# Kernel optimization log

Hardware: AMD Instinct MI355X
Metric: run time of the kernel (lower is better)

Reference implementation:

```python
import jax, jax.numpy as jnp
import numpy as np
from jax import lax

DN = ('NCHW', 'OIHW', 'NCHW')

def conv(x, w, b):
    y = lax.conv_general_dilated(x, w, (1, 1), 'VALID', dimension_numbers=DN)
    return y + b[None, :, None, None]

def maxpool2(x):
    return lax.reduce_window(x, -jnp.inf, lax.max, (1, 1, 2, 2), (1, 1, 2, 2), 'VALID')

def setup_inputs() -> dict:
    key = jax.random.key(0)
    ks = jax.random.split(key, 16)
    s = 0.05
    return {
        'x': jax.random.normal(ks[0], (8192, 1, 28, 28), jnp.float32),
        'kf_w1': jax.random.normal(ks[1], (8, 1, 7, 7), jnp.float32) * s,
        'kf_b1': jax.random.normal(ks[2], (8,), jnp.float32) * s,
        'kf_w2': jax.random.normal(ks[3], (10, 8, 5, 5), jnp.float32) * s,
        'kf_b2': jax.random.normal(ks[4], (10,), jnp.float32) * s,
        'kf_fc1_w': jax.random.normal(ks[5], (32, 90), jnp.float32) * s,
        'kf_fc1_b': jax.random.normal(ks[6], (32,), jnp.float32) * s,
        'kf_fc2_w': jax.random.normal(ks[7], (40, 32), jnp.float32) * s,
        'kf_fc2_b': jax.random.normal(ks[8], (40,), jnp.float32) * s,
        'conv2_w': jax.random.normal(ks[9], (20, 10, 5, 5), jnp.float32) * s,
        'conv2_b': jax.random.normal(ks[10], (20,), jnp.float32) * s,
        'fc1_w': jax.random.normal(ks[11], (50, 320), jnp.float32) * s,
        'fc1_b': jax.random.normal(ks[12], (50,), jnp.float32) * s,
        'fc2_w': jax.random.normal(ks[13], (10, 50), jnp.float32) * s,
        'fc2_b': jax.random.normal(ks[14], (10,), jnp.float32) * s,
    }

def _forward(x, kf_w1, kf_b1, kf_w2, kf_b2, kf_fc1_w, kf_fc1_b, kf_fc2_w, kf_fc2_b,
             conv2_w, conv2_b, fc1_w, fc1_b, fc2_w, fc2_b):
    n = x.shape[0]
    # KernelFinder: conv7 -> pool -> relu -> conv5 -> pool -> relu
    f = jax.nn.relu(maxpool2(conv(x, kf_w1, kf_b1)))        # [N,8,11,11]
    f = jax.nn.relu(maxpool2(conv(f, kf_w2, kf_b2)))        # [N,10,3,3]
    f = f.reshape(n, 90)
    h = jax.nn.relu(f @ kf_fc1_w.T + kf_fc1_b)
    kernels = (h @ kf_fc2_w.T + kf_fc2_b).reshape(n, 10, 1, 2, 2)
    # per-sample dynamic conv: each image gets its own [10,1,2,2] kernel
    def one(img, k):
        return lax.conv_general_dilated(img[None], k, (1, 1), 'VALID',
                                        dimension_numbers=DN)[0]
    y = jax.vmap(one)(x, kernels)                           # [N,10,27,27]
    y = jax.nn.relu(maxpool2(y))                            # [N,10,13,13]
    # dropout2d is identity in eval mode
    y = jax.nn.relu(maxpool2(conv(y, conv2_w, conv2_b)))    # [N,20,4,4]
    y = y.reshape(n, 320)
    y = jax.nn.relu(y @ fc1_w.T + fc1_b)
    # F.dropout identity in eval
    y = y @ fc2_w.T + fc2_b
    return jax.nn.log_softmax(y, axis=1)

def reference(x, kf_w1, kf_b1, kf_w2, kf_b2, kf_fc1_w, kf_fc1_b, kf_fc2_w, kf_fc2_b,
              conv2_w, conv2_b, fc1_w, fc1_b, fc2_w, fc2_b):
    return _forward(x, kf_w1, kf_b1, kf_w2, kf_b2, kf_fc1_w, kf_fc1_b, kf_fc2_w,
                    kf_fc2_b, conv2_w, conv2_b, fc1_w, fc1_b, fc2_w, fc2_b)
```

## Files before the change

kernel.cpp:

```cpp
#include <hip/hip_runtime.h>
#include <math.h>

#define TPB 192

typedef __attribute__((ext_vector_type(8))) short bf16x8;
typedef __attribute__((ext_vector_type(4))) float f32x4;

#define OX    0
#define OXB   784
#define OC7   2720
#define OC1B  5024
#define OC5   784
#define OY2   784
#define OC2S  2720
#define OF    5552
#define OH    5644
#define OK2   5676
#define OP3   0
#define OPF   320
#define OA1   420
#define OZ    472
#define SM_TOT 5716

#define W3U 0
#define W5U 9600
#define W7U 13184
#define WSU_TOT 14208

__device__ __forceinline__ unsigned short f2bf(float f) {
    unsigned int u = __float_as_uint(f);
    u += 0x7FFF + ((u >> 16) & 1);
    return (unsigned short)(u >> 16);
}

__global__ void repack_w(const float* __restrict__ conv2_w,
                         const float* __restrict__ kf_w2,
                         const float* __restrict__ kf_w1,
                         unsigned short* __restrict__ ws)
{
    int i = blockIdx.x * blockDim.x + threadIdx.x;
    if (i < 9600) {
        int g = i / 640, rem = i % 640;
        int oc = rem >> 5, k = rem & 31;
        int kyp = g % 3, kx = g / 3;
        int kyip = k >> 4, ic = k & 15, ky = 2 * kyp + kyip;
        float v = 0.f;
        if (ic < 10 && ky < 5)
            v = conv2_w[(oc * 10 + ic) * 25 + ky * 5 + kx];
        ws[W3U + i] = f2bf(v);
    } else if (i < 13184) {
        int j = i - 9600;
        int s = j >> 9, rem = j & 511;
        int oc = rem >> 5, k = rem & 31;
        int tap = 4 * s + (k >> 3), ic = k & 7;
        float v = 0.f;
        if (oc < 10 && tap < 25)
            v = kf_w2[(oc * 8 + ic) * 25 + tap];
        ws[W5U + j] = f2bf(v);
    } else if (i < WSU_TOT) {
        int j = i - 13184;
        int s = j >> 9, oc = (j >> 5) & 15, k = j & 31;
        int ky = s * 4 + (k >> 3), kx = k & 7;
        float v = 0.f;
        if (oc < 8 && kx < 7 && ky < 7)
            v = kf_w1[oc * 49 + ky * 7 + kx];
        ws[W7U + j] = f2bf(v);
    }
}

__global__ __launch_bounds__(TPB) void fused_forward(
    const float* __restrict__ x,
    const float* __restrict__ kf_w1, const float* __restrict__ kf_b1,
    const float* __restrict__ kf_w2, const float* __restrict__ kf_b2,
    const float* __restrict__ kf_fc1_w, const float* __restrict__ kf_fc1_b,
    const float* __restrict__ kf_fc2_w, const float* __restrict__ kf_fc2_b,
    const float* __restrict__ conv2_w, const float* __restrict__ conv2_b,
    const float* __restrict__ fc1_w, const float* __restrict__ fc1_b,
    const float* __restrict__ fc2_w, const float* __restrict__ fc2_b,
    const unsigned short* __restrict__ wsu,
    float* __restrict__ out)
{
    __shared__ __align__(16) float sm[SM_TOT];
    const int tid = threadIdx.x;
    const int n = blockIdx.x;

    const float bias1 = kf_b1[tid & 7];
    const int l  = tid & 63, wv = tid >> 6;
    const int lm = l & 15, lk = l >> 4;

    bf16x8 A7_0, A7_1;
    {
        const unsigned short* W7 = wsu + W7U;
        A7_0 = *(const bf16x8*)(W7 + lm * 32 + lk * 8);
        A7_1 = *(const bf16x8*)(W7 + 512 + lm * 32 + lk * 8);
    }

    {
        const float4* xg = (const float4*)(x + (long long)n * 784);
        float4* d = (float4*)&sm[OX];
        for (int i = tid; i < 196; i += TPB) d[i] = xg[i];
    }
    __syncthreads();

    {
        unsigned short* xb = (unsigned short*)&sm[OXB];
        #pragma unroll
        for (int i = 0; i < 20; ++i) {
            int e = i * 192 + tid;
            int s = e / 960, rem = e - s * 960;
            int r = rem >> 5, m = rem & 31;
            int c = m + s;
            float v = (r < 28 && c < 28) ? sm[OX + r * 28 + c] : 0.f;
            xb[s * 968 + rem] = f2bf(v);
        }
    }
    __syncthreads();

    for (int g = 0; g < 3; ++g) {
        {
            const unsigned short* xb = (const unsigned short*)&sm[OXB];
            float* C7 = &sm[OC7];
            #pragma unroll
            for (int j = 0; j < 4; ++j) {
                int nn = (wv * 4 + j) * 16 + lm;
                int lr = nn / 24, c = nn - lr * 24;
                int s = c & 3, q = c - s;
                f32x4 acc = {0.f, 0.f, 0.f, 0.f};
                #pragma unroll
                for (int s4 = 0; s4 < 2; ++s4) {
                    int rb = 8 * g + lr + s4 * 4 + lk;
                    rb = rb > 29 ? 29 : rb;
                    const unsigned short* p = xb + s * 968 + rb * 32 + q;
                    short4 lo = *(const short4*)p;
                    short4 hi = *(const short4*)(p + 4);
                    bf16x8 B;
                    B[0] = lo.x; B[1] = lo.y; B[2] = lo.z; B[3] = lo.w;
                    B[4] = hi.x; B[5] = hi.y; B[6] = hi.z; B[7] = hi.w;
                    acc = __builtin_amdgcn_mfma_f32_16x16x32_bf16(
                        s4 ? A7_1 : A7_0, B, acc, 0, 0, 0);
                }
                if (lk < 2)
                    *(f32x4*)(C7 + nn * 12 + lk * 4) = acc;
            }
        }
        __syncthreads();

        if (tid < 176) {
            int oc = tid & 7, qq = tid >> 3;
            int c = qq % 11, plr2 = qq / 11;
            const float* C7 = &sm[OC7];
            unsigned short* c1b = (unsigned short*)&sm[OC1B];
            #pragma unroll
            for (int hh = 0; hh < 2; ++hh) {
                int plr = plr2 + 2 * hh;
                int p = 4 * g + plr;
                if (p < 11) {
                    int nb = (2 * plr) * 24 + 2 * c;
                    float v00 = C7[nb * 12 + oc];
                    float v01 = C7[(nb + 1) * 12 + oc];
                    float v10 = C7[(nb + 24) * 12 + oc];
                    float v11 = C7[(nb + 25) * 12 + oc];
                    float m = fmaxf(fmaxf(v00, v01), fmaxf(v10, v11)) + bias1;
                    c1b[p * 96 + c * 8 + oc] = f2bf(fmaxf(m, 0.f));
                }
            }
        }
        __syncthreads();
    }

    {
        int nn = wv * 16 + lm;
        int nc = nn > 35 ? 35 : nn;
        const int rr = nc / 6, cc = nc - rr * 6;
        const unsigned short* c1b = (const unsigned short*)&sm[OC1B];
        const char* W5 = (const char*)(wsu + W5U);
        f32x4 acc = {0.f, 0.f, 0.f, 0.f};
        #pragma unroll
        for (int s = 0; s < 7; ++s) {
            int tap = 4 * s + lk;
            int ky = (tap * 13) >> 6;
            int kx = tap - ky * 5;
            bf16x8 A = *(const bf16x8*)(W5 + s * 1024 + lm * 64 + lk * 16);
            bf16x8 B = *(const bf16x8*)(c1b + (rr + ky) * 96 + (cc + kx) * 8);
            acc = __builtin_amdgcn_mfma_f32_16x16x32_bf16(A, B, acc, 0, 0, 0);
        }
        *(f32x4*)(&sm[OC5] + nn * 20 + lk * 4) = acc;
    }
    __syncthreads();

    if (tid < 90) {
        int oc = tid % 10, rr = tid / 10;
        int py = rr / 3, px = rr % 3;
        const float* C5 = &sm[OC5];
        int nb = (2 * py) * 6 + 2 * px;
        float v = fmaxf(fmaxf(C5[nb * 20 + oc], C5[(nb + 1) * 20 + oc]),
                        fmaxf(C5[(nb + 6) * 20 + oc], C5[(nb + 7) * 20 + oc]));
        sm[OF + oc * 9 + rr] = fmaxf(v + kf_b2[oc], 0.f);
    }
    __syncthreads();

    if (tid < 32) {
        float acc = kf_fc1_b[tid];
        const float2* wr = (const float2*)&kf_fc1_w[tid * 90];
        const float2* ff = (const float2*)&sm[OF];
        for (int i = 0; i < 45; ++i) {
            float2 wv2 = wr[i], fv = ff[i];
            acc = fmaf(wv2.x, fv.x, acc);
            acc = fmaf(wv2.y, fv.y, acc);
        }
        sm[OH + tid] = fmaxf(acc, 0.f);
    }
    if (tid < 40) {
        float acc = kf_fc2_b[tid];
        const float4* wr = (const float4*)&kf_fc2_w[tid * 32];
        const float4* hh = (const float4*)&sm[OH];
        #pragma unroll
        for (int i = 0; i < 8; ++i) {
            float4 wv2 = wr[i], hv = hh[i];
            acc = fmaf(wv2.x, hv.x, acc);
            acc = fmaf(wv2.y, hv.y, acc);
            acc = fmaf(wv2.z, hv.z, acc);
            acc = fmaf(wv2.w, hv.w, acc);
        }
        sm[OK2 + tid] = acc;
    }
    if (tid >= 64) {
        float4* z4 = (float4*)&sm[OY2];
        for (int i = tid - 64; i < 468; i += 128) z4[i] = float4{0.f, 0.f, 0.f, 0.f};
    }
    __syncthreads();

    if (tid < 120) {
        int oc = tid % 10, py = tid / 10;
        float4 kv = *(const float4*)&sm[OK2 + oc * 4];
        float k0 = kv.x, k1 = kv.y, k2 = kv.z, k3 = kv.w;
        const float* x0 = &sm[OX + 2 * py * 28];
        const float* x1 = x0 + 28;
        const float* x2 = x0 + 56;
        float2 q0 = *(const float2*)&x0[0];
        float2 q1 = *(const float2*)&x1[0];
        float2 q2 = *(const float2*)&x2[0];
        float A0 = q0.x, B0 = q0.y;
        float A1 = q1.x, B1 = q1.y;
        float A2 = q2.x, B2 = q2.y;
        unsigned short* y2 = (unsigned short*)&sm[OY2];
        #pragma unroll
        for (int j = 0; j < 12; ++j) {
            float2 r0 = *(const float2*)&x0[2 * j + 2];
            float2 r1 = *(const float2*)&x1[2 * j + 2];
            float2 r2v = *(const float2*)&x2[2 * j + 2];
            float C0 = r0.x, C1 = r1.x, C2 = r2v.x;
            float c00 = A0 * k0 + B0 * k1 + A1 * k2 + B1 * k3;
            float c01 = B0 * k0 + C0 * k1 + B1 * k2 + C1 * k3;
            float c10 = A1 * k0 + B1 * k1 + A2 * k2 + B2 * k3;
            float c11 = B1 * k0 + C1 * k1 + B2 * k2 + C2 * k3;
            float m = fmaxf(fmaxf(c00, c01), fmaxf(c10, c11));
            y2[py * 288 + j * 24 + oc] = f2bf(fmaxf(m, 0.f));
            A0 = C0; A1 = C1; A2 = C2;
            B0 = r0.y; B1 = r1.y; B2 = r2v.y;
        }
    }
    __syncthreads();

    if (wv < 2) {
        f32x4 a00 = {0.f, 0.f, 0.f, 0.f};
        f32x4 a01 = a00, a10 = a00, a11 = a00;
        const char* W3 = (const char*)(wsu + W3U);
        const int aoff0 = lm * 64 + lk * 16;
        const int oc1 = 16 + (lm < 4 ? lm : 3);
        const int aoff1 = oc1 * 64 + lk * 16;
        const int n0 = wv * 32 + lm;
        const int n1 = n0 + 16;
        const int kyip = l >> 5, icb = (lk & 1) * 8;
        const unsigned short* Y2 = (const unsigned short*)&sm[OY2];
        const int b0 = ((n0 >> 3) + kyip) * 288 + (n0 & 7) * 24 + icb;
        const int b1 = ((n1 >> 3) + kyip) * 288 + (n1 & 7) * 24 + icb;
        #pragma unroll
        for (int p = 0; p < 3; ++p) {
            #pragma unroll
            for (int kx = 0; kx < 5; ++kx) {
                const char* wa = W3 + (kx * 3 + p) * 1280;
                bf16x8 A0 = *(const bf16x8*)(wa + aoff0);
                bf16x8 A1 = *(const bf16x8*)(wa + aoff1);
                const int bo = p * 576 + kx * 24;
                bf16x8 B0 = *(const bf16x8*)(Y2 + b0 + bo);
                bf16x8 B1 = *(const bf16x8*)(Y2 + b1 + bo);
                a00 = __builtin_amdgcn_mfma_f32_16x16x32_bf16(A0, B0, a00, 0, 0, 0);
                a01 = __builtin_amdgcn_mfma_f32_16x16x32_bf16(A0, B1, a01, 0, 0, 0);
                a10 = __builtin_amdgcn_mfma_f32_16x16x32_bf16(A1, B0, a10, 0, 0, 0);
                a11 = __builtin_amdgcn_mfma_f32_16x16x32_bf16(A1, B1, a11, 0, 0, 0);
            }
        }
        float* C = &sm[OC2S];
        *(f32x4*)(C + n0 * 36 + lk * 4)      = a00;
        *(f32x4*)(C + n1 * 36 + lk * 4)      = a01;
        *(f32x4*)(C + n0 * 36 + 16 + lk * 4) = a10;
        *(f32x4*)(C + n1 * 36 + 16 + lk * 4) = a11;
    }
    __syncthreads();

    if (tid < 80) {
        int oc = tid % 20, py = tid / 20;
        float b = conv2_b[oc];
        const float* C = &sm[OC2S];
        #pragma unroll
        for (int px = 0; px < 4; ++px) {
            int n00 = (2 * py) * 8 + 2 * px;
            float c00 = C[n00 * 36 + oc];
            float c01 = C[(n00 + 1) * 36 + oc];
            float c10 = C[(n00 + 8) * 36 + oc];
            float c11 = C[(n00 + 9) * 36 + oc];
            float m = fmaxf(fmaxf(c00, c01), fmaxf(c10, c11)) + b;
            sm[OP3 + oc * 16 + py * 4 + px] = fmaxf(m, 0.f);
        }
    }
    __syncthreads();

    if (tid < 100) {
        int g = tid / 50, o = tid % 50;
        const float4* wr4 = (const float4*)&fc1_w[o * 320 + g * 160];
        const float4* pp4 = (const float4*)&sm[OP3 + g * 160];
        float acc = 0.f;
        for (int i = 0; i < 40; ++i) {
            float4 wv2 = wr4[i], pv = pp4[i];
            acc = fmaf(wv2.x, pv.x, acc);
            acc = fmaf(wv2.y, pv.y, acc);
            acc = fmaf(wv2.z, pv.z, acc);
            acc = fmaf(wv2.w, pv.w, acc);
        }
        sm[OPF + tid] = acc;
    }
    __syncthreads();

    if (tid < 50) {
        float acc = fc1_b[tid] + sm[OPF + tid] + sm[OPF + 50 + tid];
        sm[OA1 + tid] = fmaxf(acc, 0.f);
    }
    if (tid < 10) {
        float acc = fc2_b[tid];
        const float2* wr = (const float2*)&fc2_w[tid * 50];
        #pragma unroll
        for (int i = 0; i < 25; ++i) {
            float2 wv2 = wr[i];
            acc = fmaf(wv2.x, sm[OA1 + 2 * i], acc);
            acc = fmaf(wv2.y, sm[OA1 + 2 * i + 1], acc);
        }
        sm[OZ + tid] = acc;
    }
    if (tid < 10) {
        float m = sm[OZ + 0];
        #pragma unroll
        for (int i = 1; i < 10; ++i) m = fmaxf(m, sm[OZ + i]);
        float s = 0.f;
        #pragma unroll
        for (int i = 0; i < 10; ++i) s += expf(sm[OZ + i] - m);
        out[n * 10 + tid] = sm[OZ + tid] - m - logf(s);
    }
}

extern "C" void kernel_launch(void* const* d_in, const int* in_sizes, int n_in,
                              void* d_out, int out_size, void* d_ws, size_t ws_size,
                              hipStream_t stream) {
    const float* x        = (const float*)d_in[0];
    const float* kf_w1    = (const float*)d_in[1];
    const float* kf_b1    = (const float*)d_in[2];
    const float* kf_w2    = (const float*)d_in[3];
    const float* kf_b2    = (const float*)d_in[4];
    const float* kf_fc1_w = (const float*)d_in[5];
    const float* kf_fc1_b = (const float*)d_in[6];
    const float* kf_fc2_w = (const float*)d_in[7];
    const float* kf_fc2_b = (const float*)d_in[8];
    const float* conv2_w  = (const float*)d_in[9];
    const float* conv2_b  = (const float*)d_in[10];
    const float* fc1_w    = (const float*)d_in[11];
    const float* fc1_b    = (const float*)d_in[12];
    const float* fc2_w    = (const float*)d_in[13];
    const float* fc2_b    = (const float*)d_in[14];

    const int N = in_sizes[0] / 784;

    unsigned short* wsu = (unsigned short*)d_ws;
    repack_w<<<(WSU_TOT + 255) / 256, 256, 0, stream>>>(conv2_w, kf_w2, kf_w1, wsu);

    fused_forward<<<N, TPB, 0, stream>>>(
        x, kf_w1, kf_b1, kf_w2, kf_b2, kf_fc1_w, kf_fc1_b, kf_fc2_w, kf_fc2_b,
        conv2_w, conv2_b, fc1_w, fc1_b, fc2_w, fc2_b, wsu, (float*)d_out);
}
```

Baseline: 217.7 us.

## Fuse maxpool into MFMA epilogues via DPP lane shuffles, drop conv staging buffers

The MFMA column mapping for conv7 and conv5 is reordered so that the four outputs of each 2x2 pool window land in neighbouring lanes (lane xor 1 and xor 8). Pooling then uses DPP max shuffles in registers, with bias, ReLU and bf16 packing applied before results are written straight to shared memory. This removes the C7/C5 staging buffers, the separate pooling passes and several __syncthreads per group, and it shrinks shared memory use, which may raise occupancy. The risk is in the more intricate lane-to-output mapping and in guard conditions that leave some lanes idle.

New measurement: 221.4 us. About the same (+1.7%).

```diff
diff --git a/kernel.cpp b/kernel.cpp
--- a/kernel.cpp
+++ b/kernel.cpp
@@ -8,19 +8,17 @@
 
 #define OX    0
 #define OXB   784
-#define OC7   2720
-#define OC1B  5024
-#define OC5   784
+#define OC1B  2720
 #define OY2   784
+#define OF    3248
+#define OH    3340
+#define OK2   3372
 #define OC2S  2720
-#define OF    5552
-#define OH    5644
-#define OK2   5676
 #define OP3   0
 #define OPF   320
 #define OA1   420
 #define OZ    472
-#define SM_TOT 5716
+#define SM_TOT 5024
 
 #define W3U 0
 #define W5U 9600
@@ -31,6 +29,17 @@
     unsigned int u = __float_as_uint(f);
     u += 0x7FFF + ((u >> 16) & 1);
     return (unsigned short)(u >> 16);
+}
+
+__device__ __forceinline__ float dppmax1(float v) {
+    float o = __int_as_float(__builtin_amdgcn_mov_dpp(
+        __float_as_int(v), 0xB1, 0xF, 0xF, true));
+    return fmaxf(v, o);
+}
+__device__ __forceinline__ float dppmax8(float v) {
+    float o = __int_as_float(__builtin_amdgcn_mov_dpp(
+        __float_as_int(v), 0x128, 0xF, 0xF, true));
+    return fmaxf(v, o);
 }
 
 __global__ void repack_w(const float* __restrict__ conv2_w,
@@ -84,7 +93,6 @@
     const int tid = threadIdx.x;
     const int n = blockIdx.x;
 
-    const float bias1 = kf_b1[tid & 7];
     const int l  = tid & 63, wv = tid >> 6;
     const int lm = l & 15, lk = l >> 4;
 
@@ -94,6 +102,7 @@
         A7_0 = *(const bf16x8*)(W7 + lm * 32 + lk * 8);
         A7_1 = *(const bf16x8*)(W7 + 512 + lm * 32 + lk * 8);
     }
+    float4 b1v = *(const float4*)(kf_b1 + (lk < 2 ? lk : 0) * 4);
 
     {
         const float4* xg = (const float4*)(x + (long long)n * 784);
@@ -116,15 +125,16 @@
     }
     __syncthreads();
 
-    for (int g = 0; g < 3; ++g) {
-        {
-            const unsigned short* xb = (const unsigned short*)&sm[OXB];
-            float* C7 = &sm[OC7];
+    {
+        const unsigned short* xb = (const unsigned short*)&sm[OXB];
+        unsigned short* c1b = (unsigned short*)&sm[OC1B];
+        for (int g = 0; g < 3; ++g) {
             #pragma unroll
             for (int j = 0; j < 4; ++j) {
-                int nn = (wv * 4 + j) * 16 + lm;
-                int lr = nn / 24, c = nn - lr * 24;
-                int s = c & 3, q = c - s;
+                int t = wv * 4 + j;
+                int C = 2 * t + (lm >> 3);
+                int lr = lm & 7;
+                int s = C & 3, q = C - s;
                 f32x4 acc = {0.f, 0.f, 0.f, 0.f};
                 #pragma unroll
                 for (int s4 = 0; s4 < 2; ++s4) {
@@ -139,39 +149,28 @@
                     acc = __builtin_amdgcn_mfma_f32_16x16x32_bf16(
                         s4 ? A7_1 : A7_0, B, acc, 0, 0, 0);
                 }
-                if (lk < 2)
-                    *(f32x4*)(C7 + nn * 12 + lk * 4) = acc;
-            }
-        }
-        __syncthreads();
-
-        if (tid < 176) {
-            int oc = tid & 7, qq = tid >> 3;
-            int c = qq % 11, plr2 = qq / 11;
-            const float* C7 = &sm[OC7];
-            unsigned short* c1b = (unsigned short*)&sm[OC1B];
-            #pragma unroll
-            for (int hh = 0; hh < 2; ++hh) {
-                int plr = plr2 + 2 * hh;
-                int p = 4 * g + plr;
-                if (p < 11) {
-                    int nb = (2 * plr) * 24 + 2 * c;
-                    float v00 = C7[nb * 12 + oc];
-                    float v01 = C7[(nb + 1) * 12 + oc];
-                    float v10 = C7[(nb + 24) * 12 + oc];
-                    float v11 = C7[(nb + 25) * 12 + oc];
-                    float m = fmaxf(fmaxf(v00, v01), fmaxf(v10, v11)) + bias1;
-                    c1b[p * 96 + c * 8 + oc] = f2bf(fmaxf(m, 0.f));
+                #pragma unroll
+                for (int e = 0; e < 4; ++e) acc[e] = dppmax1(acc[e]);
+                #pragma unroll
+                for (int e = 0; e < 4; ++e) acc[e] = dppmax8(acc[e]);
+                int pr = 4 * g + (lm >> 1);
+                if ((lm & 1) == 0 && lm < 8 && lk < 2 && t < 11 && pr < 11) {
+                    short4 w;
+                    w.x = (short)f2bf(fmaxf(acc[0] + b1v.x, 0.f));
+                    w.y = (short)f2bf(fmaxf(acc[1] + b1v.y, 0.f));
+                    w.z = (short)f2bf(fmaxf(acc[2] + b1v.z, 0.f));
+                    w.w = (short)f2bf(fmaxf(acc[3] + b1v.w, 0.f));
+                    *(short4*)(c1b + pr * 96 + t * 8 + lk * 4) = w;
                 }
             }
         }
-        __syncthreads();
-    }
-
-    {
-        int nn = wv * 16 + lm;
-        int nc = nn > 35 ? 35 : nn;
-        const int rr = nc / 6, cc = nc - rr * 6;
+    }
+    __syncthreads();
+
+    {
+        int row = lm & 7;
+        int colc = 2 * wv + (lm >> 3);
+        int rowc = row > 5 ? 5 : row;
         const unsigned short* c1b = (const unsigned short*)&sm[OC1B];
         const char* W5 = (const char*)(wsu + W5U);
         f32x4 acc = {0.f, 0.f, 0.f, 0.f};
@@ -181,21 +180,28 @@
             int ky = (tap * 13) >> 6;
             int kx = tap - ky * 5;
             bf16x8 A = *(const bf16x8*)(W5 + s * 1024 + lm * 64 + lk * 16);
-            bf16x8 B = *(const bf16x8*)(c1b + (rr + ky) * 96 + (cc + kx) * 8);
+            bf16x8 B = *(const bf16x8*)(c1b + (rowc + ky) * 96 + (colc + kx) * 8);
             acc = __builtin_amdgcn_mfma_f32_16x16x32_bf16(A, B, acc, 0, 0, 0);
         }
-        *(f32x4*)(&sm[OC5] + nn * 20 + lk * 4) = acc;
-    }
-    __syncthreads();
-
-    if (tid < 90) {
-        int oc = tid % 10, rr = tid / 10;
-        int py = rr / 3, px = rr % 3;
-        const float* C5 = &sm[OC5];
-        int nb = (2 * py) * 6 + 2 * px;
-        float v = fmaxf(fmaxf(C5[nb * 20 + oc], C5[(nb + 1) * 20 + oc]),
-                        fmaxf(C5[(nb + 6) * 20 + oc], C5[(nb + 7) * 20 + oc]));
-        sm[OF + oc * 9 + rr] = fmaxf(v + kf_b2[oc], 0.f);
+        #pragma unroll
+        for (int e = 0; e < 4; ++e) acc[e] = dppmax1(acc[e]);
+        #pragma unroll
+        for (int e = 0; e < 4; ++e) acc[e] = dppmax8(acc[e]);
+        if ((lm & 1) == 0 && lm < 6 && lk < 3) {
+            int py = lm >> 1, px = wv;
+            float* f = &sm[OF];
+            if (lk < 2) {
+                float4 b2 = *(const float4*)(kf_b2 + lk * 4);
+                f[(lk * 4 + 0) * 9 + py * 3 + px] = fmaxf(acc[0] + b2.x, 0.f);
+                f[(lk * 4 + 1) * 9 + py * 3 + px] = fmaxf(acc[1] + b2.y, 0.f);
+                f[(lk * 4 + 2) * 9 + py * 3 + px] = fmaxf(acc[2] + b2.z, 0.f);
+                f[(lk * 4 + 3) * 9 + py * 3 + px] = fmaxf(acc[3] + b2.w, 0.f);
+            } else {
+                float2 b2 = *(const float2*)(kf_b2 + 8);
+                f[8 * 9 + py * 3 + px] = fmaxf(acc[0] + b2.x, 0.f);
+                f[9 * 9 + py * 3 + px] = fmaxf(acc[1] + b2.y, 0.f);
+            }
+        }
     }
     __syncthreads();
 
```
